# Kernel optimization log

Measured on AMD Instinct MI355X. Metric: run time of the kernel, lower is better.

The kernel has to match this reference:

```python
import jax, jax.numpy as jnp
import numpy as np

N = 20000        # number of graph nodes (objects + regions)
E = 660000       # number of directed edges (~avg degree 33)
F_DIM = 254      # feature_dims = in_feats // 2
IN_FEATS = 508   # (256 - 2) * 2
GLOVE = 300


def _gcn_layer(x, W, b, src, dst, norm_src, norm_dst):
    """DGL GraphConv, norm='both'. W: [in, out], b: [out]."""
    n = x.shape[0]
    pre_mult = W.shape[0] > W.shape[1]  # DGL applies W first if in > out
    if pre_mult:
        x = x @ W
    h = (x * norm_src[:, None])[src]                      # [E, F] gather
    agg = jax.ops.segment_sum(h, dst, num_segments=n)     # scatter-add [N, F]
    agg = agg * norm_dst[:, None]
    if not pre_mult:
        agg = agg @ W
    return agg + b


def setup_inputs() -> dict:
    key = jax.random.key(0)
    ks = jax.random.split(key, 12)
    w = lambda k, shape: jax.random.normal(k, shape, jnp.float32) * 0.02
    return {
        "class_embed": jax.random.normal(ks[0], (N,), jnp.float32),
        "all_glove": jax.random.normal(ks[1], (N, GLOVE), jnp.float32),
        "W_word": w(ks[2], (F_DIM, GLOVE)),
        "b_word": jnp.zeros((F_DIM,), jnp.float32),
        "W_img": w(ks[3], (F_DIM, N)),
        "b_img": jnp.zeros((F_DIM,), jnp.float32),
        "W1": w(ks[4], (IN_FEATS, IN_FEATS)),
        "b1": jnp.zeros((IN_FEATS,), jnp.float32),
        "W2": w(ks[5], (IN_FEATS, IN_FEATS)),
        "b2": jnp.zeros((IN_FEATS,), jnp.float32),
        "W3": w(ks[6], (IN_FEATS, 1)),
        "b3": jnp.zeros((1,), jnp.float32),
        "W_fin": w(ks[7], (F_DIM, N)),
        "b_fin": jnp.zeros((F_DIM,), jnp.float32),
        "src": jax.random.randint(ks[8], (E,), 0, N, jnp.int32),
        "dst": jax.random.randint(ks[9], (E,), 0, N, jnp.int32),
    }


def reference(class_embed, all_glove, W_word, b_word, W_img, b_img,
              W1, b1, W2, b2, W3, b3, W_fin, b_fin, src, dst):
    n = all_glove.shape[0]
    ones = jnp.ones(src.shape, jnp.float32)
    deg_out = jax.ops.segment_sum(ones, src, num_segments=n)
    deg_in = jax.ops.segment_sum(ones, dst, num_segments=n)
    # norm='both': zero where degree is zero (DGL replaces inf with 0)
    norm_src = jnp.where(deg_out > 0, jnp.maximum(deg_out, 1.0) ** -0.5, 0.0)
    norm_dst = jnp.where(deg_in > 0, jnp.maximum(deg_in, 1.0) ** -0.5, 0.0)

    ce = class_embed.reshape(1, -1) @ W_img.T + b_img      # [1, 254]
    we = all_glove @ W_word.T + b_word                     # [N, 254]
    x = jnp.concatenate([jnp.broadcast_to(ce, (n, F_DIM)), we], axis=1)  # [N, 508]

    h = jax.nn.relu(_gcn_layer(x, W1, b1, src, dst, norm_src, norm_dst))
    h = jax.nn.relu(_gcn_layer(h, W2, b2, src, dst, norm_src, norm_dst))
    o = jax.nn.relu(_gcn_layer(h, W3, b3, src, dst, norm_src, norm_dst))  # [N, 1]

    return o.reshape(1, -1) @ W_fin.T + b_fin              # [1, 254]
```

## Files before the change

kernel.cpp:

```cpp
#include <hip/hip_runtime.h>
#include <hip/hip_bf16.h>

#define TPB 256
#define NB_E 32
#define HTPB 512
#define NHALF_LDS 10240

typedef __attribute__((ext_vector_type(8))) short bf16x8_t;
typedef __attribute__((ext_vector_type(4))) float f32x4_t;
typedef __attribute__((ext_vector_type(8))) unsigned short u16x8_t;
typedef __attribute__((ext_vector_type(4))) unsigned short u16x4_t;

__device__ __forceinline__ float bf2f(unsigned short u) {
    return __uint_as_float(((unsigned)u) << 16);
}
__device__ __forceinline__ unsigned short f2bf(float f) {
    unsigned x = __float_as_uint(f);
    unsigned r = (x + 0x7fff + ((x >> 16) & 1)) >> 16;
    return (unsigned short)r;
}

__device__ __forceinline__ void gload16(const unsigned short* g, unsigned short* l) {
    __builtin_amdgcn_global_load_lds(
        (const __attribute__((address_space(1))) unsigned int*)(const void*)g,
        (__attribute__((address_space(3))) unsigned int*)(void*)l, 16, 0, 0);
}


__global__ __launch_bounds__(HTPB) void hist_kernel(
    const int* __restrict__ src, const int* __restrict__ dst,
    int* __restrict__ histD, int* __restrict__ histS,
    int E, int N, int nhalf, int chunk) {
    __shared__ int h[NHALF_LDS];
    int b = blockIdx.x, var = blockIdx.y;
    const int* arr = (var < 2) ? dst : src;
    int lo = (var & 1) * nhalf;
    int hi = min(lo + nhalf, N);
    int cnt = hi - lo;
    for (int i = threadIdx.x; i < cnt; i += HTPB) h[i] = 0;
    __syncthreads();
    int beg = b * chunk, end = min(E, beg + chunk);
    for (int i = beg + threadIdx.x; i < end; i += HTPB) {
        int v = arr[i];
        if (v >= lo && v < hi) atomicAdd(&h[v - lo], 1);
    }
    __syncthreads();
    int* out = ((var < 2) ? histD : histS) + (size_t)b * N + lo;
    for (int i = threadIdx.x; i < cnt; i += HTPB) out[i] = h[i];
}

__global__ void degreduce_kernel(const int* __restrict__ histD, const int* __restrict__ histS,
                                 float* __restrict__ ns, float* __restrict__ nd,
                                 int* __restrict__ degp, int N) {
    int n = blockIdx.x * blockDim.x + threadIdx.x;
    if (n >= N) return;
    int di = 0, dout = 0;
    for (int b = 0; b < NB_E; b++) {
        di += histD[(size_t)b * N + n];
        dout += histS[(size_t)b * N + n];
    }
    nd[n] = di > 0 ? rsqrtf((float)di) : 0.f;
    ns[n] = dout > 0 ? rsqrtf((float)dout) : 0.f;
    degp[n] = (di + 7) & ~7;
}

__global__ __launch_bounds__(1024) void scan1(const int* __restrict__ degp,
                                              int* __restrict__ rp, int* __restrict__ bsum, int n) {
    __shared__ int buf[1024];
    int b = blockIdx.x;
    int i = b * 1024 + threadIdx.x;
    int v = (i < n) ? degp[i] : 0;
    buf[threadIdx.x] = v;
    __syncthreads();
    for (int off = 1; off < 1024; off <<= 1) {
        int t = (threadIdx.x >= off) ? buf[threadIdx.x - off] : 0;
        __syncthreads();
        buf[threadIdx.x] += t;
        __syncthreads();
    }
    if (i < n) rp[i + 1] = buf[threadIdx.x];
    if (threadIdx.x == 1023) bsum[b] = buf[1023];
    if (b == 0 && threadIdx.x == 0) rp[0] = 0;
}

__global__ void scan2(int* __restrict__ bsum, int nb) {
    int lane = threadIdx.x;
    int v = (lane < nb) ? bsum[lane] : 0;
    for (int off = 1; off < 64; off <<= 1) {
        int t = __shfl_up(v, off);
        if (lane >= off) v += t;
    }
    if (lane < nb) bsum[lane] = v;
}

__global__ __launch_bounds__(1024) void scan3(int* __restrict__ rp, const int* __restrict__ bsum, int n) {
    int b = blockIdx.x;
    if (b == 0) return;
    int i = b * 1024 + threadIdx.x;
    if (i < n) rp[i + 1] += bsum[b - 1];
}

__global__ void gbase_kernel(const int* __restrict__ histD, const int* __restrict__ rp,
                             int* __restrict__ gbase, int N) {
    int n = blockIdx.x * blockDim.x + threadIdx.x;
    if (n >= N) return;
    int run = rp[n];
    for (int b = 0; b < NB_E; b++) {
        gbase[(size_t)b * N + n] = run;
        run += histD[(size_t)b * N + n];
    }
}

__global__ __launch_bounds__(HTPB) void scatter2_kernel(
    const int* __restrict__ src, const int* __restrict__ dst,
    const int* __restrict__ gbase, const float* __restrict__ ns,
    int2* __restrict__ payload, int E, int N, int nhalf, int chunk) {
    __shared__ int h[NHALF_LDS];
    int b = blockIdx.x, half = blockIdx.y;
    int lo = half * nhalf;
    int hi = min(lo + nhalf, N);
    int cnt = hi - lo;
    for (int i = threadIdx.x; i < cnt; i += HTPB) h[i] = 0;
    __syncthreads();
    int beg = b * chunk, end = min(E, beg + chunk);
    for (int i = beg + threadIdx.x; i < end; i += HTPB) {
        int d = dst[i];
        if (d >= lo && d < hi) {
            int s = src[i];
            int rank = atomicAdd(&h[d - lo], 1);
            int pos = gbase[(size_t)b * N + d] + rank;
            payload[pos] = make_int2(s, __float_as_int(ns[s]));
        }
    }
}

__global__ __launch_bounds__(256) void st_kernel(const int* __restrict__ rp,
                                                 const int2* __restrict__ payload,
                                                 const float* __restrict__ nd,
                                                 float* __restrict__ tv, int n) {
    int d = blockIdx.x * 4 + (threadIdx.x >> 6);
    if (d >= n) return;
    int lane = threadIdx.x & 63;
    int beg = rp[d], end = rp[d + 1];
    float acc = 0.f;
    for (int e = beg + lane; e < end; e += 64) acc += __int_as_float(payload[e].y);
    for (int off = 32; off > 0; off >>= 1) acc += __shfl_down(acc, off);
    if (lane == 0) tv[d] = acc * nd[d];
}


__global__ void gemv_rows_split(const float* __restrict__ vec, const float* __restrict__ Mat,
                                const float* __restrict__ bias, float* __restrict__ out,
                                int n, int nslices) {
    int j = blockIdx.x, slice = blockIdx.y;
    int len = (n + nslices - 1) / nslices;
    int beg = slice * len, end = min(n, beg + len);
    const float* row = Mat + (size_t)j * n;
    float s = 0.f;
    for (int i = beg + threadIdx.x; i < end; i += blockDim.x) s += vec[i] * row[i];
    __shared__ float red[TPB];
    red[threadIdx.x] = s;
    __syncthreads();
    for (int o = TPB / 2; o > 0; o >>= 1) {
        if (threadIdx.x < o) red[threadIdx.x] += red[threadIdx.x + o];
        __syncthreads();
    }
    if (threadIdx.x == 0) {
        float v = red[0] + ((slice == 0 && bias) ? bias[j] : 0.f);
        atomicAdd(&out[j], v);
    }
}

__global__ __launch_bounds__(64) void u_kernel(const float* __restrict__ ce, const float* __restrict__ W1,
                                               float* __restrict__ u, int FD, int IF) {
    int j = blockIdx.x;
    int lane = threadIdx.x;
    float s = 0.f;
    for (int i = lane; i < FD; i += 64) s += ce[i] * W1[(size_t)i * IF + j];
    for (int off = 32; off > 0; off >>= 1) s += __shfl_down(s, off);
    if (lane == 0) u[j] = s;
}


__global__ void pad_convert4(const float* __restrict__ in, int icols, int irows,
                             unsigned short* __restrict__ out, int ocols, int orows, int cpr) {
    int idx = blockIdx.x * blockDim.x + threadIdx.x;
    int row = idx / cpr;
    int c4 = (idx - row * cpr) * 4;
    if (row >= orows) return;
    float4 v = make_float4(0.f, 0.f, 0.f, 0.f);
    if (row < irows && c4 < icols)
        v = *(const float4*)(in + (size_t)row * icols + c4);
    u16x4_t o;
    o[0] = f2bf(v.x); o[1] = f2bf(v.y); o[2] = f2bf(v.z); o[3] = f2bf(v.w);
    *(u16x4_t*)(out + (size_t)row * ocols + c4) = o;
}

__global__ void transpose_pad(const float* __restrict__ W, int rows, int cols, int ldw,
                              unsigned short* __restrict__ out, int orows, int ocols) {
    __shared__ float tile[32][33];
    int k0 = blockIdx.x * 32, n0 = blockIdx.y * 32;
    int tx = threadIdx.x, ty = threadIdx.y;
    for (int i = 0; i < 32; i += 8) {
        int k = k0 + ty + i, n = n0 + tx;
        tile[ty + i][tx] = (k < rows && n < cols) ? W[(size_t)k * ldw + n] : 0.f;
    }
    __syncthreads();
    for (int i = 0; i < 32; i += 8) {
        int n = n0 + ty + i, k = k0 + tx;
        if (n < orows && k < ocols) out[(size_t)n * ocols + k] = f2bf(tile[tx][ty + i]);
    }
}

__global__ __launch_bounds__(256) void mfma_gemm(
    const unsigned short* __restrict__ A, const unsigned short* __restrict__ Bt,
    const float* __restrict__ bias, const float* __restrict__ rowscale,
    const float* __restrict__ tvec, const float* __restrict__ uvec,
    const float* __restrict__ w3, float* __restrict__ zout,
    unsigned short* __restrict__ C, int M, int Nn, int Kp, int Cld, int relu) {
    __shared__ unsigned short As[2][64 * 32];
    __shared__ unsigned short Bs[2][64 * 32];
    int tid = threadIdx.x;
    int lane = tid & 63;
    int wave = tid >> 6;
    int wm = wave >> 1, wn = wave & 1;
    int lg = lane >> 4, lt = lane & 15;

    int nwg = gridDim.x * gridDim.y;
    int hid = blockIdx.y * gridDim.x + blockIdx.x;
    int q = nwg >> 3, r8 = nwg & 7;
    int xcd = hid & 7, pos = hid >> 3;
    int wg = (xcd < r8 ? xcd * (q + 1) : r8 * (q + 1) + (xcd - r8) * q) + pos;
    int row0 = (wg / gridDim.x) * 64, col0 = (wg % gridDim.x) * 64;

    f32x4_t acc[2][2] = {};

    int sr = tid >> 2, sc = tid & 3;
    int ssw = sc ^ ((sr >> 1) & 3);
    const unsigned short* gA = A + (size_t)(row0 + sr) * Kp + (ssw << 3);
    const unsigned short* gB = Bt + (size_t)(col0 + sr) * Kp + (ssw << 3);

    int nk = Kp >> 5;
    gload16(gA, As[0] + tid * 8);
    gload16(gB, Bs[0] + tid * 8);
    __syncthreads();

    int cur = 0;
    for (int kp = 0; kp < nk; kp++) {
        if (kp + 1 < nk) {
            int k0 = (kp + 1) << 5;
            gload16(gA + k0, As[cur ^ 1] + tid * 8);
            gload16(gB + k0, Bs[cur ^ 1] + tid * 8);
        }
        bf16x8_t af[2], bfr[2];
#pragma unroll
        for (int mi = 0; mi < 2; mi++) {
            int r = wm * 32 + mi * 16 + lt;
            int sw = lg ^ ((r >> 1) & 3);
            af[mi] = *(const bf16x8_t*)(As[cur] + r * 32 + sw * 8);
        }
#pragma unroll
        for (int ni = 0; ni < 2; ni++) {
            int r = wn * 32 + ni * 16 + lt;
            int sw = lg ^ ((r >> 1) & 3);
            bfr[ni] = *(const bf16x8_t*)(Bs[cur] + r * 32 + sw * 8);
        }
#pragma unroll
        for (int mi = 0; mi < 2; mi++)
#pragma unroll
            for (int ni = 0; ni < 2; ni++)
                acc[mi][ni] = __builtin_amdgcn_mfma_f32_16x16x32_bf16(af[mi], bfr[ni], acc[mi][ni], 0, 0, 0);
        __syncthreads();
        cur ^= 1;
    }

#pragma unroll
    for (int mi = 0; mi < 2; mi++) {
#pragma unroll
        for (int r = 0; r < 4; r++) {
            int row = row0 + wm * 32 + mi * 16 + lg * 4 + r;
            if (row >= M) continue;
            float rs = rowscale ? rowscale[row] : 1.f;
            float tvr = tvec ? tvec[row] : 0.f;
            float zp = 0.f;
#pragma unroll
            for (int ni = 0; ni < 2; ni++) {
                int colb = col0 + wn * 32 + ni * 16 + lt;
                float v = 0.f;
                if (colb < Nn) {
                    v = acc[mi][ni][r] * rs;
                    if (bias) v += bias[colb];
                    if (tvec) v += tvr * uvec[colb];
                    if (relu) v = fmaxf(v, 0.f);
                    if (w3) zp += v * w3[colb];
                }
                if (C) C[(size_t)row * Cld + colb] = f2bf(v);
            }
            if (w3) {
                zp += __shfl_xor(zp, 1);
                zp += __shfl_xor(zp, 2);
                zp += __shfl_xor(zp, 4);
                zp += __shfl_xor(zp, 8);
                if (lt == 0) atomicAdd(&zout[row], zp);
            }
        }
    }
}

__global__ __launch_bounds__(256) void spmm_bf16_cols(
    const int* __restrict__ rp, const int2* __restrict__ payload,
    const unsigned short* __restrict__ X, unsigned short* __restrict__ Y,
    int n, int ld, int c0) {
    int node = blockIdx.x * 4 + (threadIdx.x >> 6);
    if (node >= n) return;
    int lane = threadIdx.x & 63;
    const unsigned short* Xo = X + c0 + lane * 4;
    int beg = rp[node], end = rp[node + 1];
    float acc[4] = {};
    for (int e = beg; e < end; e += 8) {
        int2 p[8];
#pragma unroll
        for (int j = 0; j < 8; j++) p[j] = payload[e + j];
        u16x4_t v[8];
#pragma unroll
        for (int j = 0; j < 8; j++) v[j] = *(const u16x4_t*)(Xo + (size_t)p[j].x * ld);
#pragma unroll
        for (int j = 0; j < 8; j++) {
            float w = __int_as_float(p[j].y);
#pragma unroll
            for (int c = 0; c < 4; c++) acc[c] += w * bf2f(v[j][c]);
        }
    }
    u16x4_t o;
#pragma unroll
    for (int c = 0; c < 4; c++) o[c] = f2bf(acc[c]);
    *(u16x4_t*)(Y + (size_t)node * ld + c0 + lane * 4) = o;
}


__global__ __launch_bounds__(256) void z_gather(const int* __restrict__ rp,
                                                const int2* __restrict__ payload,
                                                const float* __restrict__ z,
                                                const float* __restrict__ nd, const float* __restrict__ b3,
                                                float* __restrict__ o, int n) {
    int d = blockIdx.x * 4 + (threadIdx.x >> 6);
    if (d >= n) return;
    int lane = threadIdx.x & 63;
    int beg = rp[d], end = rp[d + 1];
    float acc = 0.f;
    for (int e = beg + lane; e < end; e += 64) {
        int2 p = payload[e];
        acc += __int_as_float(p.y) * z[p.x];
    }
    for (int off = 32; off > 0; off >>= 1) acc += __shfl_down(acc, off);
    if (lane == 0) o[d] = fmaxf(nd[d] * acc + b3[0], 0.f);
}


extern "C" void kernel_launch(void* const* d_in, const int* in_sizes, int n_in,
                              void* d_out, int out_size, void* d_ws, size_t ws_size,
                              hipStream_t stream) {
    const float* class_embed = (const float*)d_in[0];
    const float* all_glove   = (const float*)d_in[1];
    const float* W_word = (const float*)d_in[2];
    const float* b_word = (const float*)d_in[3];
    const float* W_img  = (const float*)d_in[4];
    const float* b_img  = (const float*)d_in[5];
    const float* W1 = (const float*)d_in[6];
    const float* b1 = (const float*)d_in[7];
    const float* W2 = (const float*)d_in[8];
    const float* b2 = (const float*)d_in[9];
    const float* W3 = (const float*)d_in[10];
    const float* b3 = (const float*)d_in[11];
    const float* W_fin = (const float*)d_in[12];
    const float* b_fin = (const float*)d_in[13];
    const int* src = (const int*)d_in[14];
    const int* dst = (const int*)d_in[15];

    const int N   = in_sizes[0];
    const int GLV = in_sizes[1] / N;
    const int FD  = in_sizes[5];
    const int IF  = in_sizes[7];
    const int E   = in_sizes[14];

    const int GLVp = 320;
    const int FDp  = 256;
    const int IFp  = 512;
    const int Mp   = (N + 63) & ~63;
    const int EP   = E + 8 * N;
    const int nhalf = (N + 1) / 2;
    const int chunk = (E + NB_E - 1) / NB_E;

    char* base = (char*)d_ws;
    size_t off = 0;
    auto alloc = [&](size_t bytes) -> void* {
        void* p = base + off;
        off = (off + bytes + 255) & ~(size_t)255;
        return p;
    };

    float* z   = (float*)alloc((size_t)N * 4);
    float* ce  = (float*)alloc((size_t)FD * 4);
    size_t zero_bytes = (size_t)((char*)(ce + FD) - (char*)z);
    float* ns  = (float*)alloc((size_t)N * 4);
    float* nd  = (float*)alloc((size_t)N * 4);
    float* tv  = (float*)alloc((size_t)N * 4);
    float* u   = (float*)alloc((size_t)IF * 4);
    float* ov  = (float*)alloc((size_t)N * 4);
    int* degp  = (int*)alloc((size_t)N * 4);
    int* rp    = (int*)alloc((size_t)(N + 1) * 4);
    int* bsum  = (int*)alloc(64 * 4);
    int* histD = (int*)alloc((size_t)NB_E * N * 4);
    int* histS = (int*)alloc((size_t)NB_E * N * 4);
    int* gbase = (int*)alloc((size_t)NB_E * N * 4);
    int2* payload = (int2*)alloc((size_t)EP * 8);
    unsigned short* WwP  = (unsigned short*)alloc((size_t)FDp * GLVp * 2);
    unsigned short* W1hT = (unsigned short*)alloc((size_t)IFp * FDp * 2);
    unsigned short* W2T  = (unsigned short*)alloc((size_t)IFp * IFp * 2);
    unsigned short* glove_bf = (unsigned short*)alloc((size_t)Mp * GLVp * 2);
    unsigned short* we       = (unsigned short*)alloc((size_t)Mp * FDp * 2);
    unsigned short* h12      = (unsigned short*)alloc((size_t)Mp * IFp * 2);
    unsigned short* aggwe = glove_bf;
    unsigned short* agg2  = glove_bf;
    unsigned short* h1 = h12;

    hipMemsetAsync(z, 0, zero_bytes, stream);
    hipMemsetAsync(payload, 0, (size_t)EP * 8, stream);
    hipMemsetAsync(d_out, 0, (size_t)FD * 4, stream);

    int gN = (N + TPB - 1) / TPB;
    int nb = (N + 1023) / 1024;

    {
        dim3 g(NB_E, 4);
        hist_kernel<<<g, HTPB, 0, stream>>>(src, dst, histD, histS, E, N, nhalf, chunk);
    }
    degreduce_kernel<<<gN, TPB, 0, stream>>>(histD, histS, ns, nd, degp, N);
    scan1<<<nb, 1024, 0, stream>>>(degp, rp, bsum, N);
    scan2<<<1, 64, 0, stream>>>(bsum, nb);
    scan3<<<nb, 1024, 0, stream>>>(rp, bsum, N);
    gbase_kernel<<<gN, TPB, 0, stream>>>(histD, rp, gbase, N);
    {
        dim3 g(NB_E, 2);
        scatter2_kernel<<<g, HTPB, 0, stream>>>(src, dst, gbase, ns, payload, E, N, nhalf, chunk);
    }
    st_kernel<<<(N + 3) / 4, 256, 0, stream>>>(rp, payload, nd, tv, N);

    {
        dim3 g(FD, 8);
        gemv_rows_split<<<g, TPB, 0, stream>>>(class_embed, W_img, b_img, ce, N, 8);
    }
    u_kernel<<<IF, 64, 0, stream>>>(ce, W1, u, FD, IF);

    {
        int cpr = GLVp / 4;
        int tot = Mp * cpr;
        pad_convert4<<<(tot + 255) / 256, 256, 0, stream>>>(all_glove, GLV, N, glove_bf, GLVp, Mp, cpr);
        int tot2 = FDp * cpr;
        pad_convert4<<<(tot2 + 255) / 256, 256, 0, stream>>>(W_word, GLV, FD, WwP, GLVp, FDp, cpr);
    }
    {
        dim3 g(FDp / 32, IFp / 32);
        transpose_pad<<<g, dim3(32, 8), 0, stream>>>(W1 + (size_t)FD * IF, FD, IF, IF, W1hT, IFp, FDp);
    }
    {
        dim3 g(IFp / 32, IFp / 32);
        transpose_pad<<<g, dim3(32, 8), 0, stream>>>(W2, IF, IF, IF, W2T, IFp, IFp);
    }

    int mtiles = Mp / 64;

    {
        dim3 g(FDp / 64, mtiles);
        mfma_gemm<<<g, 256, 0, stream>>>(glove_bf, WwP, b_word, nullptr, nullptr, nullptr,
                                         nullptr, nullptr, we, N, FD, GLVp, FDp, 0);
    }
    spmm_bf16_cols<<<(N + 3) / 4, 256, 0, stream>>>(rp, payload, we, aggwe, N, FDp, 0);
    {
        dim3 g(IFp / 64, mtiles);
        mfma_gemm<<<g, 256, 0, stream>>>(aggwe, W1hT, b1, nd, tv, u,
                                         nullptr, nullptr, h1, N, IF, FDp, IFp, 1);
    }
    spmm_bf16_cols<<<(N + 3) / 4, 256, 0, stream>>>(rp, payload, h1, agg2, N, IFp, 0);
    spmm_bf16_cols<<<(N + 3) / 4, 256, 0, stream>>>(rp, payload, h1, agg2, N, IFp, 256);
    {
        dim3 g(IFp / 64, mtiles);
        mfma_gemm<<<g, 256, 0, stream>>>(agg2, W2T, b2, nd, nullptr, nullptr,
                                         W3, z, nullptr, N, IF, IFp, IFp, 1);
    }
    z_gather<<<(N + 3) / 4, 256, 0, stream>>>(rp, payload, z, nd, b3, ov, N);
    {
        dim3 g(FD, 8);
        gemv_rows_split<<<g, TPB, 0, stream>>>(ov, W_fin, b_fin, (float*)d_out, N, 8);
    }
}
```

Measured before the change: 327.4 us.

## Pre-bucket edges by source range and fuse 512-wide SpMM into one pass

Adds a three-kernel coarse bucket sort that groups the edge list by source-node range (src>>11) before the histogram and scatter stages. Within each destination's CSR row the gathered source indices then tend to follow bucket order, which should improve cache locality of the feature-row gathers in the SpMM kernels. It also replaces the two column-half SpMM launches on the 512-wide hidden layer with one kernel where each lane loads 8 bf16 values, so payload and index reads happen once. The cost is three extra small launches plus an extra read and write pass over src and dst, and more registers per lane in the wide SpMM.

```diff
diff --git a/kernel.cpp b/kernel.cpp
--- a/kernel.cpp
+++ b/kernel.cpp
@@ -5,6 +5,8 @@
 #define NB_E 32
 #define HTPB 512
 #define NHALF_LDS 10240
+#define ASHIFT 11
+#define NBLK_A 64
 
 typedef __attribute__((ext_vector_type(8))) short bf16x8_t;
 typedef __attribute__((ext_vector_type(4))) float f32x4_t;
@@ -24,6 +26,58 @@
     __builtin_amdgcn_global_load_lds(
         (const __attribute__((address_space(1))) unsigned int*)(const void*)g,
         (__attribute__((address_space(3))) unsigned int*)(void*)l, 16, 0, 0);
+}
+
+
+__global__ __launch_bounds__(1024) void sortA_count(const int* __restrict__ src,
+                                                    int* __restrict__ cnt, int E, int nch, int chunkE) {
+    __shared__ int h[16];
+    if (threadIdx.x < 16) h[threadIdx.x] = 0;
+    __syncthreads();
+    int b = blockIdx.x;
+    int beg = b * chunkE, end = min(E, beg + chunkE);
+    for (int i = beg + threadIdx.x; i < end; i += 1024)
+        atomicAdd(&h[src[i] >> ASHIFT], 1);
+    __syncthreads();
+    if (threadIdx.x < nch) cnt[threadIdx.x * NBLK_A + b] = h[threadIdx.x];
+}
+
+__global__ __launch_bounds__(1024) void sortA_scan(int* __restrict__ cnt, int n) {
+    __shared__ int buf[1024];
+    int v = (threadIdx.x < n) ? cnt[threadIdx.x] : 0;
+    buf[threadIdx.x] = v;
+    __syncthreads();
+    for (int off = 1; off < 1024; off <<= 1) {
+        int t = (threadIdx.x >= off) ? buf[threadIdx.x - off] : 0;
+        __syncthreads();
+        buf[threadIdx.x] += t;
+        __syncthreads();
+    }
+    if (threadIdx.x < n) cnt[threadIdx.x] = buf[threadIdx.x] - v;
+}
+
+__global__ __launch_bounds__(1024) void sortA_scatter(const int* __restrict__ src,
+                                                      const int* __restrict__ dst,
+                                                      const int* __restrict__ cnt,
+                                                      int* __restrict__ src2, int* __restrict__ dst2,
+                                                      int E, int nch, int chunkE) {
+    __shared__ int base[16];
+    __shared__ int rnk[16];
+    int b = blockIdx.x;
+    if (threadIdx.x < nch) {
+        base[threadIdx.x] = cnt[threadIdx.x * NBLK_A + b];
+        rnk[threadIdx.x] = 0;
+    }
+    __syncthreads();
+    int beg = b * chunkE, end = min(E, beg + chunkE);
+    for (int i = beg + threadIdx.x; i < end; i += 1024) {
+        int s = src[i], d = dst[i];
+        int c = s >> ASHIFT;
+        int r = atomicAdd(&rnk[c], 1);
+        int pos = base[c] + r;
+        src2[pos] = s;
+        dst2[pos] = d;
+    }
 }
 
 
@@ -307,14 +361,43 @@
     }
 }
 
-__global__ __launch_bounds__(256) void spmm_bf16_cols(
+
+__global__ __launch_bounds__(256) void spmm_bf16_512(
     const int* __restrict__ rp, const int2* __restrict__ payload,
-    const unsigned short* __restrict__ X, unsigned short* __restrict__ Y,
-    int n, int ld, int c0) {
+    const unsigned short* __restrict__ X, unsigned short* __restrict__ Y, int n) {
     int node = blockIdx.x * 4 + (threadIdx.x >> 6);
     if (node >= n) return;
     int lane = threadIdx.x & 63;
-    const unsigned short* Xo = X + c0 + lane * 4;
+    const unsigned short* Xo = X + lane * 8;
+    int beg = rp[node], end = rp[node + 1];
+    float acc[8] = {};
+    for (int e = beg; e < end; e += 8) {
+        int2 p[8];
+#pragma unroll
+        for (int j = 0; j < 8; j++) p[j] = payload[e + j];
+        u16x8_t v[8];
+#pragma unroll
+        for (int j = 0; j < 8; j++) v[j] = *(const u16x8_t*)(Xo + (size_t)p[j].x * 512);
+#pragma unroll
+        for (int j = 0; j < 8; j++) {
+            float w = __int_as_float(p[j].y);
+#pragma unroll
+            for (int c = 0; c < 8; c++) acc[c] += w * bf2f(v[j][c]);
+        }
+    }
+    u16x8_t o;
+#pragma unroll
+    for (int c = 0; c < 8; c++) o[c] = f2bf(acc[c]);
+    *(u16x8_t*)(Y + (size_t)node * 512 + lane * 8) = o;
+}
+
+__global__ __launch_bounds__(256) void spmm_bf16_256(
+    const int* __restrict__ rp, const int2* __restrict__ payload,
+    const unsigned short* __restrict__ X, unsigned short* __restrict__ Y, int n) {
+    int node = blockIdx.x * 4 + (threadIdx.x >> 6);
+    if (node >= n) return;
+    int lane = threadIdx.x & 63;
+    const unsigned short* Xo = X + lane * 4;
     int beg = rp[node], end = rp[node + 1];
     float acc[4] = {};
     for (int e = beg; e < end; e += 8) {
@@ -323,7 +406,7 @@
         for (int j = 0; j < 8; j++) p[j] = payload[e + j];
         u16x4_t v[8];
 #pragma unroll
-        for (int j = 0; j < 8; j++) v[j] = *(const u16x4_t*)(Xo + (size_t)p[j].x * ld);
+        for (int j = 0; j < 8; j++) v[j] = *(const u16x4_t*)(Xo + (size_t)p[j].x * 256);
 #pragma unroll
         for (int j = 0; j < 8; j++) {
             float w = __int_as_float(p[j].y);
@@ -334,7 +417,7 @@
     u16x4_t o;
 #pragma unroll
     for (int c = 0; c < 4; c++) o[c] = f2bf(acc[c]);
-    *(u16x4_t*)(Y + (size_t)node * ld + c0 + lane * 4) = o;
+    *(u16x4_t*)(Y + (size_t)node * 256 + lane * 4) = o;
 }
 
 
@@ -390,6 +473,8 @@
     const int EP   = E + 8 * N;
     const int nhalf = (N + 1) / 2;
     const int chunk = (E + NB_E - 1) / NB_E;
+    const int nch   = (N >> ASHIFT) + 1;
+    const int chunkE = (E + NBLK_A - 1) / NBLK_A;
 
     char* base = (char*)d_ws;
     size_t off = 0;
@@ -410,6 +495,9 @@
     int* degp  = (int*)alloc((size_t)N * 4);
     int* rp    = (int*)alloc((size_t)(N + 1) * 4);
     int* bsum  = (int*)alloc(64 * 4);
+    int* acnt  = (int*)alloc((size_t)16 * NBLK_A * 4);
+    int* src2  = (int*)alloc((size_t)E * 4);
+    int* dst2  = (int*)alloc((size_t)E * 4);
     int* histD = (int*)alloc((size_t)NB_E * N * 4);
     int* histS = (int*)alloc((size_t)NB_E * N * 4);
     int* gbase = (int*)alloc((size_t)NB_E * N * 4);
@@ -431,9 +519,13 @@
     int gN = (N + TPB - 1) / TPB;
     int nb = (N + 1023) / 1024;
 
+    sortA_count<<<NBLK_A, 1024, 0, stream>>>(src, acnt, E, nch, chunkE);
+    sortA_scan<<<1, 1024, 0, stream>>>(acnt, nch * NBLK_A);
+    sortA_scatter<<<NBLK_A, 1024, 0, stream>>>(src, dst, acnt, src2, dst2, E, nch, chunkE);
+
     {
         dim3 g(NB_E, 4);
-        hist_kernel<<<g, HTPB, 0, stream>>>(src, dst, histD, histS, E, N, nhalf, chunk);
+        hist_kernel<<<g, HTPB, 0, stream>>>(src2, dst2, histD, histS, E, N, nhalf, chunk);
     }
     degreduce_kernel<<<gN, TPB, 0, stream>>>(histD, histS, ns, nd, degp, N);
     scan1<<<nb, 1024, 0, stream>>>(degp, rp, bsum, N);
@@ -442,7 +534,7 @@
     gbase_kernel<<<gN, TPB, 0, stream>>>(histD, rp, gbase, N);
     {
         dim3 g(NB_E, 2);
-        scatter2_kernel<<<g, HTPB, 0, stream>>>(src, dst, gbase, ns, payload, E, N, nhalf, chunk);
+        scatter2_kernel<<<g, HTPB, 0, stream>>>(src2, dst2, gbase, ns, payload, E, N, nhalf, chunk);
     }
     st_kernel<<<(N + 3) / 4, 256, 0, stream>>>(rp, payload, nd, tv, N);
 
@@ -475,14 +567,13 @@
         mfma_gemm<<<g, 256, 0, stream>>>(glove_bf, WwP, b_word, nullptr, nullptr, nullptr,
                                          nullptr, nullptr, we, N, FD, GLVp, FDp, 0);
     }
-    spmm_bf16_cols<<<(N + 3) / 4, 256, 0, stream>>>(rp, payload, we, aggwe, N, FDp, 0);
+    spmm_bf16_256<<<(N + 3) / 4, 256, 0, stream>>>(rp, payload, we, aggwe, N);
     {
         dim3 g(IFp / 64, mtiles);
         mfma_gemm<<<g, 256, 0, stream>>>(aggwe, W1hT, b1, nd, tv, u,
                                          nullptr, nullptr, h1, N, IF, FDp, IFp, 1);
     }
-    spmm_bf16_cols<<<(N + 3) / 4, 256, 0, stream>>>(rp, payload, h1, agg2, N, IFp, 0);
-    spmm_bf16_cols<<<(N + 3) / 4, 256, 0, stream>>>(rp, payload, h1, agg2, N, IFp, 256);
+    spmm_bf16_512<<<(N + 3) / 4, 256, 0, stream>>>(rp, payload, h1, agg2, N);
     {
         dim3 g(IFp / 64, mtiles);
         mfma_gemm<<<g, 256, 0, stream>>>(agg2, W2T, b2, nd, nullptr, nullptr,
```

Result: slower. 341.0 us (+4.2%).
